# Optimization experiments

Hardware: AMD Instinct MI355X
Metric: run time of the kernel (lower is better)

## Reference

```python
import jax, jax.numpy as jnp
import numpy as np
from jax.ops import segment_sum

N = 100000   # nodes
E = 1600000  # edges
F = 128      # node feature dim
H = 128      # hidden dim
FE = 16      # edge feature dim
G = 256      # num graphs
EPS = 1e-5   # batch-norm eps


def setup_inputs() -> dict:
    key = jax.random.key(0)
    ks = jax.random.split(key, 16)
    s = 0.05
    return {
        "x": jax.random.normal(ks[0], (N, F), jnp.float32),
        "edge_index": jax.random.randint(ks[1], (2, E), 0, N, dtype=jnp.int32),
        "edge_attr": jax.random.normal(ks[2], (E, FE), jnp.float32),
        "batch_idx": jnp.sort(jax.random.randint(ks[3], (N,), 0, G, dtype=jnp.int32)),
        # GCN layer 1
        "W_g1": jax.random.normal(ks[4], (F, H), jnp.float32) * s,
        "b_g1": jnp.zeros((H,), jnp.float32),
        "gamma1": jnp.ones((H,), jnp.float32),
        "beta1": jnp.zeros((H,), jnp.float32),
        # GCN layer 2
        "W_g2": jax.random.normal(ks[5], (H, H), jnp.float32) * s,
        "b_g2": jnp.zeros((H,), jnp.float32),
        "gamma2": jnp.ones((H,), jnp.float32),
        "beta2": jnp.zeros((H,), jnp.float32),
        # edge encoder MLP
        "W_e1": jax.random.normal(ks[6], (FE, H), jnp.float32) * s,
        "b_e1": jnp.zeros((H,), jnp.float32),
        "W_e2": jax.random.normal(ks[7], (H, H), jnp.float32) * s,
        "b_e2": jnp.zeros((H,), jnp.float32),
    }


def _gcn_bn_relu(x, src, dst, W, b, gamma, beta):
    """GCNConv (sym-normalized, self-loops) + BatchNorm1d (batch stats) + ReLU."""
    h = x @ W                                             # [N, H]
    ones = jnp.ones((E,), h.dtype)
    deg = segment_sum(ones, dst, num_segments=N) + 1.0    # self-loop degree
    dinv = jax.lax.rsqrt(deg)                             # [N]
    norm = dinv[src] * dinv[dst]                          # [E]
    agg = segment_sum(h[src] * norm[:, None], dst, num_segments=N)
    out = agg + h * (dinv * dinv)[:, None] + b            # self-loop + bias
    mu = out.mean(axis=0)
    var = out.var(axis=0)
    out = (out - mu) * jax.lax.rsqrt(var + EPS) * gamma + beta
    return jax.nn.relu(out)


def reference(x, edge_index, edge_attr, batch_idx, W_g1, b_g1, gamma1, beta1,
              W_g2, b_g2, gamma2, beta2, W_e1, b_e1, W_e2, b_e2):
    src, dst = edge_index[0], edge_index[1]
    h = _gcn_bn_relu(x, src, dst, W_g1, b_g1, gamma1, beta1)
    h = _gcn_bn_relu(h, src, dst, W_g2, b_g2, gamma2, beta2)

    # global mean pool over nodes per graph
    node_cnt = segment_sum(jnp.ones((N,), h.dtype), batch_idx, num_segments=G)
    graph_repr = segment_sum(h, batch_idx, num_segments=G) / jnp.maximum(node_cnt, 1.0)[:, None]

    # edge encoder MLP + per-graph edge mean (vectorized version of the loop)
    e = jax.nn.relu(edge_attr @ W_e1 + b_e1) @ W_e2 + b_e2   # [E, H]
    edge_batch = batch_idx[src]                              # [E]
    edge_cnt = segment_sum(jnp.ones((E,), e.dtype), edge_batch, num_segments=G)
    edge_sum = segment_sum(e, edge_batch, num_segments=G)
    edge_repr = jnp.where(edge_cnt[:, None] > 0, edge_sum / jnp.maximum(edge_cnt, 1.0)[:, None], 0.0)

    return graph_repr + edge_repr  # [G, H]
```

## Files before the change

### kernel.cpp

```cpp
#include <hip/hip_runtime.h>
#include <cstdint>

__device__ inline unsigned int bfpack2(float a, float b) {
  unsigned int ua = __float_as_uint(a), ub = __float_as_uint(b);
  ua += 0x7FFFu + ((ua >> 16) & 1u);
  ub += 0x7FFFu + ((ub >> 16) & 1u);
  return (ua >> 16) | (ub & 0xFFFF0000u);
}
__device__ inline float bflo(unsigned int u) { return __uint_as_float(u << 16); }
__device__ inline float bfhi(unsigned int u) { return __uint_as_float(u & 0xFFFF0000u); }

__global__ __launch_bounds__(256) void pre_kernel(const int* __restrict__ src,
                                                  const int* __restrict__ dst,
                                                  int* __restrict__ deg,
                                                  int* __restrict__ deg2, int nE) {
  int e = blockIdx.x * 256 + threadIdx.x;
  if (e < nE) {
    atomicAdd(&deg[dst[e]], 1);
    atomicAdd(&deg2[src[e]], 1);
  }
}

__global__ __launch_bounds__(256) void scanA_kernel(const int* __restrict__ deg,
                                                    const int* __restrict__ deg2,
                                                    int* __restrict__ rp,
                                                    int* __restrict__ rp2,
                                                    int* __restrict__ part,
                                                    int* __restrict__ part2,
                                                    int n, int nb) {
  __shared__ int sh[256];
  int b = blockIdx.x, t = threadIdx.x;
  const int* d = (b < nb) ? deg : deg2;
  int* r = (b < nb) ? rp : rp2;
  int* p = (b < nb) ? part : part2;
  int pad = (b < nb) ? 1 : 0;
  int bb = (b < nb) ? b : b - nb;
  int base = bb * 1024 + t * 4;
  int v0 = (base + 0 < n) ? d[base + 0] : 0;
  int v1 = (base + 1 < n) ? d[base + 1] : 0;
  int v2 = (base + 2 < n) ? d[base + 2] : 0;
  int v3 = (base + 3 < n) ? d[base + 3] : 0;
  if (pad) {
    v0 = (v0 + 7) & ~7; v1 = (v1 + 7) & ~7;
    v2 = (v2 + 7) & ~7; v3 = (v3 + 7) & ~7;
  }
  int ts = v0 + v1 + v2 + v3;
  sh[t] = ts;
  __syncthreads();
  for (int off = 1; off < 256; off <<= 1) {
    int x = (t >= off) ? sh[t - off] : 0;
    __syncthreads();
    sh[t] += x;
    __syncthreads();
  }
  int excl = sh[t] - ts;
  if (t == 255) p[bb] = sh[255];
  if (base + 0 < n) r[base + 0] = excl;
  if (base + 1 < n) r[base + 1] = excl + v0;
  if (base + 2 < n) r[base + 2] = excl + v0 + v1;
  if (base + 3 < n) r[base + 3] = excl + v0 + v1 + v2;
}

__global__ void scanB_kernel(int* part, int* part2, int* rp, int* rp2, int nb, int n) {
  if (threadIdx.x == 0) {
    int* p = (blockIdx.x == 0) ? part : part2;
    int* r = (blockIdx.x == 0) ? rp : rp2;
    int run = 0;
    for (int i = 0; i < nb; ++i) { int v = p[i]; p[i] = run; run += v; }
    r[n] = run;
  }
}

__global__ __launch_bounds__(256) void scanC_kernel(int* __restrict__ rp,
                                                    int* __restrict__ rp2,
                                                    const int* __restrict__ part,
                                                    const int* __restrict__ part2,
                                                    int* __restrict__ cursor,
                                                    int* __restrict__ cursor2,
                                                    const int* __restrict__ deg,
                                                    float* __restrict__ dinv, int n) {
  int i = blockIdx.x * 256 + threadIdx.x;
  if (i < n) {
    int v = rp[i] + part[i >> 10];
    rp[i] = v;
    cursor[i] = v;
    dinv[i] = rsqrtf((float)deg[i] + 1.0f);
  } else if (i < 2 * n) {
    int j = i - n;
    int v = rp2[j] + part2[j >> 10];
    rp2[j] = v;
    cursor2[j] = v;
  }
}

__global__ __launch_bounds__(256) void placepad_kernel(const int* __restrict__ src,
                                                       const int* __restrict__ dst,
                                                       const int* __restrict__ batch,
                                                       const float* __restrict__ dinv,
                                                       int* __restrict__ cursor,
                                                       int* __restrict__ cursor2,
                                                       int2* __restrict__ swv,
                                                       unsigned int* __restrict__ epk,
                                                       int* __restrict__ pos2,
                                                       const int* __restrict__ rp,
                                                       const int* __restrict__ deg,
                                                       int nE, int nN) {
  int t = blockIdx.x * 256 + threadIdx.x;
  if (t < nE) {
    int s = src[t];
    int d = dst[t];
    int p1 = atomicAdd(&cursor[d], 1);
    int2 sw; sw.x = s; sw.y = __float_as_int(dinv[s] * dinv[d]);
    swv[p1] = sw;
    int g = batch[s];
    int p2 = atomicAdd(&cursor2[s], 1);
    epk[p2] = ((unsigned int)g << 21) | (unsigned int)t;
    pos2[t] = p2;
  } else if (t < nE + nN) {
    int i = t - nE;
    int b = rp[i] + deg[i], e = rp[i + 1];
    int2 z; z.x = i; z.y = 0;
    for (int k = b; k < e; ++k) swv[k] = z;
  }
}

template <bool FUSED>
__global__ __launch_bounds__(256) void gemm128_kernel(const float* __restrict__ A,
                                                      const float* __restrict__ W,
                                                      const float* __restrict__ bs,
                                                      const float* __restrict__ bq,
                                                      const float* __restrict__ gm,
                                                      const float* __restrict__ bt,
                                                      float invN,
                                                      unsigned int* __restrict__ hpk2,
                                                      int nrows) {
  extern __shared__ float lds[];
  float* Ws = lds;
  float* xs = lds + 128 * 128;
  float* scs = xs + 16 * 128;
  float* shs = scs + 128;
  const int t = threadIdx.x;
  for (int i = t; i < (128 * 128) / 4; i += 256)
    reinterpret_cast<float4*>(Ws)[i] = reinterpret_cast<const float4*>(W)[i];
  if (FUSED && t < 128) {
    float mu = bs[t] * invN;
    float var = bq[t] * invN - mu * mu;
    float sc = gm[t] * rsqrtf(var + 1e-5f);
    scs[t] = sc;
    shs[t] = bt[t] - mu * sc;
  }
  const int wave = t >> 6, lane = t & 63;
  const size_t sbase = (size_t)(lane >> 3) * (size_t)nrows * 8 + (lane & 7);
  for (int rb = blockIdx.x * 16; rb < nrows; rb += gridDim.x * 16) {
    int nr = min(16, nrows - rb);
    __syncthreads();
    for (int i = t; i < nr * 32; i += 256) {
      float4 v = reinterpret_cast<const float4*>(A + (size_t)rb * 128)[i];
      if (FUSED) {
        float4 sc4 = reinterpret_cast<const float4*>(scs)[i & 31];
        float4 sh4 = reinterpret_cast<const float4*>(shs)[i & 31];
        v.x = fmaxf(fmaf(v.x, sc4.x, sh4.x), 0.f);
        v.y = fmaxf(fmaf(v.y, sc4.y, sh4.y), 0.f);
        v.z = fmaxf(fmaf(v.z, sc4.z, sh4.z), 0.f);
        v.w = fmaxf(fmaf(v.w, sc4.w, sh4.w), 0.f);
      }
      reinterpret_cast<float4*>(xs)[i] = v;
    }
    __syncthreads();
    float acc[4][2] = {{0.f, 0.f}, {0.f, 0.f}, {0.f, 0.f}, {0.f, 0.f}};
    const float* xw = xs + wave * 4 * 128;
#pragma unroll 4
    for (int k = 0; k < 128; ++k) {
      float w0 = Ws[k * 128 + lane];
      float w1 = Ws[k * 128 + 64 + lane];
#pragma unroll
      for (int r = 0; r < 4; ++r) {
        float a = xw[r * 128 + k];
        acc[r][0] = fmaf(a, w0, acc[r][0]);
        acc[r][1] = fmaf(a, w1, acc[r][1]);
      }
    }
#pragma unroll
    for (int r = 0; r < 4; ++r) {
      int row = rb + wave * 4 + r;
      if (row < nrows)
        hpk2[sbase + (size_t)row * 8] = bfpack2(acc[r][0], acc[r][1]);
    }
  }
}

__global__ __launch_bounds__(256) void spmm8_kernel(const unsigned int* __restrict__ hpk2,
                                                    const float* __restrict__ dinv,
                                                    const int* __restrict__ rp,
                                                    const int2* __restrict__ swv,
                                                    const float* __restrict__ bias,
                                                    float* __restrict__ outp,
                                                    float* __restrict__ bnsum,
                                                    float* __restrict__ bnsq, int nN) {
  const int lane = threadIdx.x & 63;
  const int ch = lane & 7;
  const int es = lane >> 3;
  const int slice = blockIdx.x & 7;
  const unsigned int* hs = hpk2 + (size_t)slice * (size_t)nN * 8;
  const int cb = slice * 8;
  const int wib = (int)(blockIdx.x >> 3) * 4 + (int)(threadIdx.x >> 6);
  const int nws = (int)(gridDim.x >> 3) * 4;
  const unsigned long long* swq = reinterpret_cast<const unsigned long long*>(swv);
  float b0 = bias[cb + ch], b1 = bias[64 + cb + ch];
  float s0 = 0.f, s1 = 0.f, q0 = 0.f, q1 = 0.f;
  const int half = (nN + 1) >> 1;

#define SPMM_CHUNK(J, ACC0, ACC1)                                         \
  {                                                                       \
    unsigned long long v_ = __builtin_nontemporal_load(swq + (J) + es);   \
    unsigned int pp_ = hs[(size_t)(unsigned int)v_ * 8 + ch];             \
    float ww_ = __uint_as_float((unsigned int)(v_ >> 32));                \
    ACC0 = fmaf(ww_, bflo(pp_), ACC0);                                    \
    ACC1 = fmaf(ww_, bfhi(pp_), ACC1);                                    \
  }

  for (int p = wib; p < half; p += nws) {
    const int n0 = p;
    const int n1 = p + half;
    const bool has1 = n1 < nN;
    int j0 = rp[n0];
    const int end0 = rp[n0 + 1];
    int j1 = 0, end1 = 0;
    if (has1) { j1 = rp[n1]; end1 = rp[n1 + 1]; }
    float a00 = 0.f, a01 = 0.f, b00 = 0.f, b01 = 0.f;
    float a10 = 0.f, a11 = 0.f, b10 = 0.f, b11 = 0.f;
    while (j0 + 8 < end0 && j1 + 8 < end1) {
      SPMM_CHUNK(j0, a00, a01);
      SPMM_CHUNK(j0 + 8, b00, b01);
      SPMM_CHUNK(j1, a10, a11);
      SPMM_CHUNK(j1 + 8, b10, b11);
      j0 += 16; j1 += 16;
    }
    while (j0 + 8 < end0) {
      SPMM_CHUNK(j0, a00, a01);
      SPMM_CHUNK(j0 + 8, b00, b01);
      j0 += 16;
    }
    if (j0 < end0) SPMM_CHUNK(j0, a00, a01);
    while (j1 + 8 < end1) {
      SPMM_CHUNK(j1, a10, a11);
      SPMM_CHUNK(j1 + 8, b10, b11);
      j1 += 16;
    }
    if (j1 < end1) SPMM_CHUNK(j1, a10, a11);

    a00 += b00; a01 += b01;
    a10 += b10; a11 += b11;
    a00 += __shfl_xor(a00, 8);  a01 += __shfl_xor(a01, 8);
    a10 += __shfl_xor(a10, 8);  a11 += __shfl_xor(a11, 8);
    a00 += __shfl_xor(a00, 16); a01 += __shfl_xor(a01, 16);
    a10 += __shfl_xor(a10, 16); a11 += __shfl_xor(a11, 16);
    a00 += __shfl_xor(a00, 32); a01 += __shfl_xor(a01, 32);
    a10 += __shfl_xor(a10, 32); a11 += __shfl_xor(a11, 32);
    if (es == 0) {
      {
        float dn = dinv[n0];
        float sw = dn * dn;
        unsigned int pn = hs[(size_t)n0 * 8 + ch];
        float o0 = fmaf(bflo(pn), sw, a00) + b0;
        float o1 = fmaf(bfhi(pn), sw, a01) + b1;
        __builtin_nontemporal_store(o0, &outp[(size_t)n0 * 128 + cb + ch]);
        __builtin_nontemporal_store(o1, &outp[(size_t)n0 * 128 + 64 + cb + ch]);
        s0 += o0; s1 += o1;
        q0 = fmaf(o0, o0, q0); q1 = fmaf(o1, o1, q1);
      }
      if (has1) {
        float dn = dinv[n1];
        float sw = dn * dn;
        unsigned int pn = hs[(size_t)n1 * 8 + ch];
        float o0 = fmaf(bflo(pn), sw, a10) + b0;
        float o1 = fmaf(bfhi(pn), sw, a11) + b1;
        __builtin_nontemporal_store(o0, &outp[(size_t)n1 * 128 + cb + ch]);
        __builtin_nontemporal_store(o1, &outp[(size_t)n1 * 128 + 64 + cb + ch]);
        s0 += o0; s1 += o1;
        q0 = fmaf(o0, o0, q0); q1 = fmaf(o1, o1, q1);
      }
    }
  }
#undef SPMM_CHUNK
  if (es == 0) {
    atomicAdd(&bnsum[cb + ch], s0);
    atomicAdd(&bnsum[64 + cb + ch], s1);
    atomicAdd(&bnsq[cb + ch], q0);
    atomicAdd(&bnsq[64 + cb + ch], q1);
  }
}

__global__ __launch_bounds__(256) void pool_kernel(const float* __restrict__ h,
                                                   const int* __restrict__ batch,
                                                   const float* __restrict__ bs,
                                                   const float* __restrict__ bq,
                                                   const float* __restrict__ gm,
                                                   const float* __restrict__ bt,
                                                   float invN,
                                                   float* __restrict__ gsum,
                                                   float* __restrict__ gcnt,
                                                   int nN, int chunk) {
  const int lane = threadIdx.x & 63;
  const int wid = (blockIdx.x * blockDim.x + threadIdx.x) >> 6;
  int beg = wid * chunk;
  if (beg >= nN) return;
  int end = min(nN, beg + chunk);
  const int c2 = 2 * lane;
  float mu0 = bs[c2] * invN, mu1 = bs[c2 + 1] * invN;
  float va0 = bq[c2] * invN - mu0 * mu0, va1 = bq[c2 + 1] * invN - mu1 * mu1;
  float sc0 = gm[c2] * rsqrtf(va0 + 1e-5f), sc1v = gm[c2 + 1] * rsqrtf(va1 + 1e-5f);
  float sh0 = bt[c2] - mu0 * sc0, sh1v = bt[c2 + 1] - mu1 * sc1v;
  int cur = -1;
  float a0 = 0.f, a1 = 0.f, cnt = 0.f;
  for (int n = beg; n < end; ++n) {
    int g = batch[n];
    if (g != cur) {
      if (cur >= 0) {
        atomicAdd(&gsum[cur * 128 + c2], a0);
        atomicAdd(&gsum[cur * 128 + c2 + 1], a1);
        if (lane == 0) atomicAdd(&gcnt[cur], cnt);
      }
      cur = g; a0 = 0.f; a1 = 0.f; cnt = 0.f;
    }
    float2 v = *reinterpret_cast<const float2*>(h + (size_t)n * 128 + c2);
    a0 += fmaxf(fmaf(v.x, sc0, sh0), 0.f);
    a1 += fmaxf(fmaf(v.y, sc1v, sh1v), 0.f);
    cnt += 1.f;
  }
  if (cur >= 0) {
    atomicAdd(&gsum[cur * 128 + c2], a0);
    atomicAdd(&gsum[cur * 128 + c2 + 1], a1);
    if (lane == 0) atomicAdd(&gcnt[cur], cnt);
  }
}

__global__ __launch_bounds__(256) void scatter_kernel(const float* __restrict__ ea,
                                                      const int* __restrict__ pos2,
                                                      unsigned int* __restrict__ eah, int nE) {
  int e = blockIdx.x * 256 + threadIdx.x;
  if (e < nE) {
    const float4* p = reinterpret_cast<const float4*>(ea + (size_t)e * 16);
    float4 a = p[0], b = p[1], c = p[2], d = p[3];
    uint4 o0, o1;
    o0.x = bfpack2(a.x, a.y); o0.y = bfpack2(a.z, a.w);
    o0.z = bfpack2(b.x, b.y); o0.w = bfpack2(b.z, b.w);
    o1.x = bfpack2(c.x, c.y); o1.y = bfpack2(c.z, c.w);
    o1.z = bfpack2(d.x, d.y); o1.w = bfpack2(d.z, d.w);
    int j = pos2[e];
    uint4* dst = reinterpret_cast<uint4*>(eah + (size_t)j * 8);
    dst[0] = o0;
    dst[1] = o1;
  }
}

__global__ __launch_bounds__(256) void edge6_kernel(const unsigned int* __restrict__ eah,
                                                    const unsigned int* __restrict__ epk,
                                                    const float* __restrict__ We1,
                                                    const float* __restrict__ be1,
                                                    float* __restrict__ esum,
                                                    float* __restrict__ ecnt,
                                                    int nE, int chunk) {
  const int lane = threadIdx.x & 63;
  const int wid = (blockIdx.x * 256 + threadIdx.x) >> 6;
  int beg = wid * chunk;
  if (beg >= nE) return;
  int end = min(nE, beg + chunk);
  float w0[16], w1[16];
#pragma unroll
  for (int k = 0; k < 16; ++k) {
    w0[k] = We1[k * 128 + lane];
    w1[k] = We1[k * 128 + 64 + lane];
  }
  float b0 = be1[lane], b1 = be1[64 + lane];
  int cur = -1;
  float a0 = 0.f, a1 = 0.f, cnt = 0.f;
  const uint4* rowp = reinterpret_cast<const uint4*>(eah + (size_t)beg * 8);
  uint4 q0 = rowp[0], q1 = rowp[1];
  int g = (int)(epk[beg] >> 21);
  for (int j = beg; j < end; ++j) {
    uint4 n0, n1;
    int ng = g;
    if (j + 1 < end) {
      const uint4* np = reinterpret_cast<const uint4*>(eah + (size_t)(j + 1) * 8);
      n0 = np[0];
      n1 = np[1];
      ng = (int)(epk[j + 1] >> 21);
    }
    if (g != cur) {
      if (cur >= 0) {
        atomicAdd(&esum[cur * 128 + lane], a0);
        atomicAdd(&esum[cur * 128 + 64 + lane], a1);
        if (lane == 0) atomicAdd(&ecnt[cur], cnt);
      }
      cur = g; a0 = 0.f; a1 = 0.f; cnt = 0.f;
    }
    float u0 = b0, u1 = b1;
    float f;
    f = bflo(q0.x); u0 = fmaf(f, w0[0], u0);  u1 = fmaf(f, w1[0], u1);
    f = bfhi(q0.x); u0 = fmaf(f, w0[1], u0);  u1 = fmaf(f, w1[1], u1);
    f = bflo(q0.y); u0 = fmaf(f, w0[2], u0);  u1 = fmaf(f, w1[2], u1);
    f = bfhi(q0.y); u0 = fmaf(f, w0[3], u0);  u1 = fmaf(f, w1[3], u1);
    f = bflo(q0.z); u0 = fmaf(f, w0[4], u0);  u1 = fmaf(f, w1[4], u1);
    f = bfhi(q0.z); u0 = fmaf(f, w0[5], u0);  u1 = fmaf(f, w1[5], u1);
    f = bflo(q0.w); u0 = fmaf(f, w0[6], u0);  u1 = fmaf(f, w1[6], u1);
    f = bfhi(q0.w); u0 = fmaf(f, w0[7], u0);  u1 = fmaf(f, w1[7], u1);
    f = bflo(q1.x); u0 = fmaf(f, w0[8], u0);  u1 = fmaf(f, w1[8], u1);
    f = bfhi(q1.x); u0 = fmaf(f, w0[9], u0);  u1 = fmaf(f, w1[9], u1);
    f = bflo(q1.y); u0 = fmaf(f, w0[10], u0); u1 = fmaf(f, w1[10], u1);
    f = bfhi(q1.y); u0 = fmaf(f, w0[11], u0); u1 = fmaf(f, w1[11], u1);
    f = bflo(q1.z); u0 = fmaf(f, w0[12], u0); u1 = fmaf(f, w1[12], u1);
    f = bfhi(q1.z); u0 = fmaf(f, w0[13], u0); u1 = fmaf(f, w1[13], u1);
    f = bflo(q1.w); u0 = fmaf(f, w0[14], u0); u1 = fmaf(f, w1[14], u1);
    f = bfhi(q1.w); u0 = fmaf(f, w0[15], u0); u1 = fmaf(f, w1[15], u1);
    a0 += fmaxf(u0, 0.f);
    a1 += fmaxf(u1, 0.f);
    cnt += 1.f;
    q0 = n0; q1 = n1; g = ng;
  }
  if (cur >= 0) {
    atomicAdd(&esum[cur * 128 + lane], a0);
    atomicAdd(&esum[cur * 128 + 64 + lane], a1);
    if (lane == 0) atomicAdd(&ecnt[cur], cnt);
  }
}

__global__ __launch_bounds__(128) void final_kernel(const float* __restrict__ gsum,
                                                    const float* __restrict__ gcnt,
                                                    const float* __restrict__ esum,
                                                    const float* __restrict__ ecnt,
                                                    const float* __restrict__ We2,
                                                    const float* __restrict__ be2,
                                                    float* __restrict__ out) {
  __shared__ float row[128];
  int g = blockIdx.x, c = threadIdx.x;
  row[c] = esum[g * 128 + c];
  __syncthreads();
  float acc = 0.f;
#pragma unroll 4
  for (int k = 0; k < 128; ++k) acc = fmaf(row[k], We2[k * 128 + c], acc);
  float ce = ecnt[g];
  float er = (ce > 0.f) ? (acc / ce + be2[c]) : 0.f;
  float cn = gcnt[g];
  float gr = gsum[g * 128 + c] / fmaxf(cn, 1.f);
  out[g * 128 + c] = gr + er;
}

extern "C" void kernel_launch(void* const* d_in, const int* in_sizes, int n_in,
                              void* d_out, int out_size, void* d_ws, size_t ws_size,
                              hipStream_t stream) {
  const float* x    = (const float*)d_in[0];
  const int*   ei   = (const int*)d_in[1];
  const float* ea   = (const float*)d_in[2];
  const int*   bidx = (const int*)d_in[3];
  const float* Wg1  = (const float*)d_in[4];
  const float* bg1  = (const float*)d_in[5];
  const float* gm1  = (const float*)d_in[6];
  const float* bt1  = (const float*)d_in[7];
  const float* Wg2  = (const float*)d_in[8];
  const float* bg2  = (const float*)d_in[9];
  const float* gm2  = (const float*)d_in[10];
  const float* bt2  = (const float*)d_in[11];
  const float* We1  = (const float*)d_in[12];
  const float* be1  = (const float*)d_in[13];
  const float* We2  = (const float*)d_in[14];
  const float* be2  = (const float*)d_in[15];
  float* out = (float*)d_out;

  const int N = in_sizes[3];
  const int E = in_sizes[1] / 2;
  const int G = out_size / 128;
  const int* srcp = ei;
  const int* dstp = ei + E;
  const int Epad = E + 8 * N;

  char* w = (char*)d_ws;
  auto alloc = [&](size_t b) {
    char* p = w;
    w += (b + 15) & ~(size_t)15;
    return p;
  };
  float* bufB    = (float*)alloc((size_t)N * 128 * 4);
  unsigned int* hpk2 = (unsigned int*)alloc((size_t)N * 64 * 4);
  int2*  swv     = (int2*)alloc((size_t)Epad * 8);
  unsigned int* epk = (unsigned int*)alloc((size_t)E * 4);
  int*   pos2    = (int*)alloc((size_t)E * 4);
  int*   rp      = (int*)alloc((size_t)(N + 1) * 4);
  int*   rp2     = (int*)alloc((size_t)(N + 1) * 4);
  int*   cursor  = (int*)alloc((size_t)N * 4);
  int*   cursor2 = (int*)alloc((size_t)N * 4);
  float* dinv    = (float*)alloc((size_t)N * 4);
  char* zbase = w;
  int*   deg  = (int*)alloc((size_t)N * 4);
  int*   deg2 = (int*)alloc((size_t)N * 4);
  float* bs1  = (float*)alloc(512);
  float* bq1  = (float*)alloc(512);
  float* bs2  = (float*)alloc(512);
  float* bq2  = (float*)alloc(512);
  float* gsum = (float*)alloc((size_t)G * 128 * 4);
  float* gcnt = (float*)alloc((size_t)G * 4);
  float* esum = (float*)alloc((size_t)G * 128 * 4);
  float* ecnt = (float*)alloc((size_t)G * 4);
  int*   part  = (int*)alloc(4096);
  int*   part2 = (int*)alloc(4096);
  size_t zbytes = (size_t)(w - zbase);

  unsigned int* eah = (unsigned int*)bufB;

  hipMemsetAsync(zbase, 0, zbytes, stream);

  (void)hipFuncSetAttribute((const void*)gemm128_kernel<false>,
                            hipFuncAttributeMaxDynamicSharedMemorySize, 74752);
  (void)hipFuncSetAttribute((const void*)gemm128_kernel<true>,
                            hipFuncAttributeMaxDynamicSharedMemorySize, 74752);

  pre_kernel<<<(E + 255) / 256, 256, 0, stream>>>(srcp, dstp, deg, deg2, E);
  int nb = (N + 1023) / 1024;
  scanA_kernel<<<2 * nb, 256, 0, stream>>>(deg, deg2, rp, rp2, part, part2, N, nb);
  scanB_kernel<<<2, 64, 0, stream>>>(part, part2, rp, rp2, nb, N);
  scanC_kernel<<<(2 * N + 255) / 256, 256, 0, stream>>>(rp, rp2, part, part2, cursor,
                                                        cursor2, deg, dinv, N);
  placepad_kernel<<<(E + N + 255) / 256, 256, 0, stream>>>(srcp, dstp, bidx, dinv, cursor,
                                                           cursor2, swv, epk, pos2, rp, deg,
                                                           E, N);

  const float invN = 1.0f / (float)N;

  gemm128_kernel<false><<<512, 256, 74752, stream>>>(x, Wg1, nullptr, nullptr, nullptr,
                                                     nullptr, 0.f, hpk2, N);
  spmm8_kernel<<<2048, 256, 0, stream>>>(hpk2, dinv, rp, swv, bg1, bufB, bs1, bq1, N);

  gemm128_kernel<true><<<512, 256, 74752, stream>>>(bufB, Wg2, bs1, bq1, gm1, bt1, invN,
                                                    hpk2, N);
  spmm8_kernel<<<2048, 256, 0, stream>>>(hpk2, dinv, rp, swv, bg2, bufB, bs2, bq2, N);

  int nwp = (2048 * 256) / 64;
  int chunkN = (N + nwp - 1) / nwp;
  pool_kernel<<<2048, 256, 0, stream>>>(bufB, bidx, bs2, bq2, gm2, bt2, invN,
                                        gsum, gcnt, N, chunkN);

  scatter_kernel<<<(E + 255) / 256, 256, 0, stream>>>(ea, pos2, eah, E);
  int nwe = (2048 * 256) / 64;
  int chunkE = (E + nwe - 1) / nwe;
  edge6_kernel<<<2048, 256, 0, stream>>>(eah, epk, We1, be1, esum, ecnt, E, chunkE);

  final_kernel<<<G, 128, 0, stream>>>(gsum, gcnt, esum, ecnt, We2, be2, out);
}
```

Measured before the change: 1.270 ms.

## Fuse edge-attr bf16 scatter into placepad and software-pipeline SpMM index loads

The placepad kernel now converts edge attributes to bf16 and writes them straight to their src-sorted slot in a dedicated buffer, when the workspace has room. This removes the separate scatter kernel and the pos2 round trip. The SpMM main loop is software-pipelined: it prefetches the next iteration's (index, weight) pairs before the FMAs, so load latency overlaps with compute. The prefetch can read past the end of the array, so 32 extra zeroed padding slots are added to swv. The cost is a larger workspace and extra register pressure in the SpMM.

```diff
diff --git a/kernel.cpp b/kernel.cpp
--- a/kernel.cpp
+++ b/kernel.cpp
@@ -93,15 +93,18 @@
   }
 }
 
+template <bool SC>
 __global__ __launch_bounds__(256) void placepad_kernel(const int* __restrict__ src,
                                                        const int* __restrict__ dst,
                                                        const int* __restrict__ batch,
                                                        const float* __restrict__ dinv,
+                                                       const float* __restrict__ ea,
                                                        int* __restrict__ cursor,
                                                        int* __restrict__ cursor2,
                                                        int2* __restrict__ swv,
                                                        unsigned int* __restrict__ epk,
                                                        int* __restrict__ pos2,
+                                                       unsigned int* __restrict__ eah,
                                                        const int* __restrict__ rp,
                                                        const int* __restrict__ deg,
                                                        int nE, int nN) {
@@ -115,12 +118,30 @@
     int g = batch[s];
     int p2 = atomicAdd(&cursor2[s], 1);
     epk[p2] = ((unsigned int)g << 21) | (unsigned int)t;
-    pos2[t] = p2;
+    if (SC) {
+      const float4* p = reinterpret_cast<const float4*>(ea + (size_t)t * 16);
+      float4 a = p[0], b = p[1], c = p[2], dd = p[3];
+      uint4 o0, o1;
+      o0.x = bfpack2(a.x, a.y); o0.y = bfpack2(a.z, a.w);
+      o0.z = bfpack2(b.x, b.y); o0.w = bfpack2(b.z, b.w);
+      o1.x = bfpack2(c.x, c.y); o1.y = bfpack2(c.z, c.w);
+      o1.z = bfpack2(dd.x, dd.y); o1.w = bfpack2(dd.z, dd.w);
+      uint4* dp = reinterpret_cast<uint4*>(eah + (size_t)p2 * 8);
+      dp[0] = o0;
+      dp[1] = o1;
+    } else {
+      pos2[t] = p2;
+    }
   } else if (t < nE + nN) {
     int i = t - nE;
     int b = rp[i] + deg[i], e = rp[i + 1];
-    int2 z; z.x = i; z.y = 0;
+    int2 z; z.x = 0; z.y = 0;
+    z.x = i;
     for (int k = b; k < e; ++k) swv[k] = z;
+  } else if (t < nE + nN + 32) {
+    int k = t - nE - nN;
+    int2 z; z.x = 0; z.y = 0;
+    swv[rp[nN] + k] = z;
   }
 }
 
@@ -218,6 +239,12 @@
     ACC0 = fmaf(ww_, bflo(pp_), ACC0);                                    \
     ACC1 = fmaf(ww_, bfhi(pp_), ACC1);                                    \
   }
+#define SPMM_FMA(V, P, ACC0, ACC1)                                        \
+  {                                                                       \
+    float ww_ = __uint_as_float((unsigned int)((V) >> 32));               \
+    ACC0 = fmaf(ww_, bflo(P), ACC0);                                      \
+    ACC1 = fmaf(ww_, bfhi(P), ACC1);                                      \
+  }
 
   for (int p = wib; p < half; p += nws) {
     const int n0 = p;
@@ -229,12 +256,27 @@
     if (has1) { j1 = rp[n1]; end1 = rp[n1 + 1]; }
     float a00 = 0.f, a01 = 0.f, b00 = 0.f, b01 = 0.f;
     float a10 = 0.f, a11 = 0.f, b10 = 0.f, b11 = 0.f;
-    while (j0 + 8 < end0 && j1 + 8 < end1) {
-      SPMM_CHUNK(j0, a00, a01);
-      SPMM_CHUNK(j0 + 8, b00, b01);
-      SPMM_CHUNK(j1, a10, a11);
-      SPMM_CHUNK(j1 + 8, b10, b11);
+    unsigned long long v0 = __builtin_nontemporal_load(swq + j0 + es);
+    unsigned long long v1 = __builtin_nontemporal_load(swq + j0 + 8 + es);
+    unsigned long long v2 = __builtin_nontemporal_load(swq + j1 + es);
+    unsigned long long v3 = __builtin_nontemporal_load(swq + j1 + 8 + es);
+    bool run = (j0 + 8 < end0) && (j1 + 8 < end1);
+    while (run) {
+      unsigned int p0 = hs[(size_t)(unsigned int)v0 * 8 + ch];
+      unsigned int p1 = hs[(size_t)(unsigned int)v1 * 8 + ch];
+      unsigned int p2 = hs[(size_t)(unsigned int)v2 * 8 + ch];
+      unsigned int p3 = hs[(size_t)(unsigned int)v3 * 8 + ch];
       j0 += 16; j1 += 16;
+      unsigned long long n0v = __builtin_nontemporal_load(swq + j0 + es);
+      unsigned long long n1v = __builtin_nontemporal_load(swq + j0 + 8 + es);
+      unsigned long long n2v = __builtin_nontemporal_load(swq + j1 + es);
+      unsigned long long n3v = __builtin_nontemporal_load(swq + j1 + 8 + es);
+      SPMM_FMA(v0, p0, a00, a01);
+      SPMM_FMA(v1, p1, b00, b01);
+      SPMM_FMA(v2, p2, a10, a11);
+      SPMM_FMA(v3, p3, b10, b11);
+      v0 = n0v; v1 = n1v; v2 = n2v; v3 = n3v;
+      run = (j0 + 8 < end0) && (j1 + 8 < end1);
     }
     while (j0 + 8 < end0) {
       SPMM_CHUNK(j0, a00, a01);
@@ -283,6 +325,7 @@
     }
   }
 #undef SPMM_CHUNK
+#undef SPMM_FMA
   if (es == 0) {
     atomicAdd(&bnsum[cb + ch], s0);
     atomicAdd(&bnsum[64 + cb + ch], s1);
@@ -482,7 +525,7 @@
   };
   float* bufB    = (float*)alloc((size_t)N * 128 * 4);
   unsigned int* hpk2 = (unsigned int*)alloc((size_t)N * 64 * 4);
-  int2*  swv     = (int2*)alloc((size_t)Epad * 8);
+  int2*  swv     = (int2*)alloc(((size_t)Epad + 32) * 8);
   unsigned int* epk = (unsigned int*)alloc((size_t)E * 4);
   int*   pos2    = (int*)alloc((size_t)E * 4);
   int*   rp      = (int*)alloc((size_t)(N + 1) * 4);
@@ -505,7 +548,10 @@
   int*   part2 = (int*)alloc(4096);
   size_t zbytes = (size_t)(w - zbase);
 
-  unsigned int* eah = (unsigned int*)bufB;
+  size_t used = (size_t)(w - (char*)d_ws);
+  size_t eah_bytes = (size_t)E * 32;
+  bool dedicated = (used + eah_bytes + 64) <= ws_size;
+  unsigned int* eah = dedicated ? (unsigned int*)alloc(eah_bytes) : (unsigned int*)bufB;
 
   hipMemsetAsync(zbase, 0, zbytes, stream);
 
@@ -520,9 +566,16 @@
   scanB_kernel<<<2, 64, 0, stream>>>(part, part2, rp, rp2, nb, N);
   scanC_kernel<<<(2 * N + 255) / 256, 256, 0, stream>>>(rp, rp2, part, part2, cursor,
                                                         cursor2, deg, dinv, N);
-  placepad_kernel<<<(E + N + 255) / 256, 256, 0, stream>>>(srcp, dstp, bidx, dinv, cursor,
-                                                           cursor2, swv, epk, pos2, rp, deg,
-                                                           E, N);
+  int ppg = (E + N + 32 + 255) / 256;
+  if (dedicated) {
+    placepad_kernel<true><<<ppg, 256, 0, stream>>>(srcp, dstp, bidx, dinv, ea, cursor,
+                                                   cursor2, swv, epk, pos2, eah, rp, deg,
+                                                   E, N);
+  } else {
+    placepad_kernel<false><<<ppg, 256, 0, stream>>>(srcp, dstp, bidx, dinv, ea, cursor,
+                                                    cursor2, swv, epk, pos2, eah, rp, deg,
+                                                    E, N);
+  }
 
   const float invN = 1.0f / (float)N;
 
@@ -539,7 +592,9 @@
   pool_kernel<<<2048, 256, 0, stream>>>(bufB, bidx, bs2, bq2, gm2, bt2, invN,
                                         gsum, gcnt, N, chunkN);
 
-  scatter_kernel<<<(E + 255) / 256, 256, 0, stream>>>(ea, pos2, eah, E);
+  if (!dedicated) {
+    scatter_kernel<<<(E + 255) / 256, 256, 0, stream>>>(ea, pos2, eah, E);
+  }
   int nwe = (2048 * 256) / 64;
   int chunkE = (E + nwe - 1) / nwe;
   edge6_kernel<<<2048, 256, 0, stream>>>(eah, epk, We1, be1, esum, ecnt, E, chunkE);
```

Measured after the change: 1.257 ms. No clear change (-1.0%).

## Pack CSR entries into 32 bits and fuse edge-attr scatter into placement

Applied to the files above, without the earlier changes.

CSR edge entries move from an 8-byte (src, fp32 weight) pair to one 32-bit word holding a 17-bit source index and a 15-bit truncated bf16 weight, halving index traffic in both SpMM passes. When the workspace has room, edge attributes are converted to bf16 and written directly to their sorted positions inside the placement kernel, so the separate scatter kernel and the pos2 round trip are dropped. This lowers the precision of the normalization weights and limits node count to 2^17. The dedicated path also needs a larger workspace.

```diff
diff --git a/kernel.cpp b/kernel.cpp
--- a/kernel.cpp
+++ b/kernel.cpp
@@ -93,15 +93,18 @@
   }
 }
 
+template <bool SC>
 __global__ __launch_bounds__(256) void placepad_kernel(const int* __restrict__ src,
                                                        const int* __restrict__ dst,
                                                        const int* __restrict__ batch,
                                                        const float* __restrict__ dinv,
+                                                       const float* __restrict__ ea,
                                                        int* __restrict__ cursor,
                                                        int* __restrict__ cursor2,
-                                                       int2* __restrict__ swv,
+                                                       unsigned int* __restrict__ swp,
                                                        unsigned int* __restrict__ epk,
                                                        int* __restrict__ pos2,
+                                                       unsigned int* __restrict__ eah,
                                                        const int* __restrict__ rp,
                                                        const int* __restrict__ deg,
                                                        int nE, int nN) {
@@ -110,17 +113,33 @@
     int s = src[t];
     int d = dst[t];
     int p1 = atomicAdd(&cursor[d], 1);
-    int2 sw; sw.x = s; sw.y = __float_as_int(dinv[s] * dinv[d]);
-    swv[p1] = sw;
+    unsigned int fb = __float_as_uint(dinv[s] * dinv[d]);
+    fb += 0x7FFFu + ((fb >> 16) & 1u);
+    swp[p1] = ((fb >> 16) << 17) | (unsigned int)s;
     int g = batch[s];
     int p2 = atomicAdd(&cursor2[s], 1);
     epk[p2] = ((unsigned int)g << 21) | (unsigned int)t;
-    pos2[t] = p2;
+    if (SC) {
+      const float4* p = reinterpret_cast<const float4*>(ea + (size_t)t * 16);
+      float4 a = p[0], b = p[1], c = p[2], dd = p[3];
+      uint4 o0, o1;
+      o0.x = bfpack2(a.x, a.y); o0.y = bfpack2(a.z, a.w);
+      o0.z = bfpack2(b.x, b.y); o0.w = bfpack2(b.z, b.w);
+      o1.x = bfpack2(c.x, c.y); o1.y = bfpack2(c.z, c.w);
+      o1.z = bfpack2(dd.x, dd.y); o1.w = bfpack2(dd.z, dd.w);
+      uint4* dp = reinterpret_cast<uint4*>(eah + (size_t)p2 * 8);
+      dp[0] = o0;
+      dp[1] = o1;
+    } else {
+      pos2[t] = p2;
+    }
   } else if (t < nE + nN) {
     int i = t - nE;
     int b = rp[i] + deg[i], e = rp[i + 1];
-    int2 z; z.x = i; z.y = 0;
-    for (int k = b; k < e; ++k) swv[k] = z;
+    for (int k = b; k < e; ++k) swp[k] = (unsigned int)i;
+  } else if (t < nE + nN + 32) {
+    int k = t - nE - nN;
+    swp[rp[nN] + k] = 0u;
   }
 }
 
@@ -192,7 +211,7 @@
 __global__ __launch_bounds__(256) void spmm8_kernel(const unsigned int* __restrict__ hpk2,
                                                     const float* __restrict__ dinv,
                                                     const int* __restrict__ rp,
-                                                    const int2* __restrict__ swv,
+                                                    const unsigned int* __restrict__ swp,
                                                     const float* __restrict__ bias,
                                                     float* __restrict__ outp,
                                                     float* __restrict__ bnsum,
@@ -205,16 +224,15 @@
   const int cb = slice * 8;
   const int wib = (int)(blockIdx.x >> 3) * 4 + (int)(threadIdx.x >> 6);
   const int nws = (int)(gridDim.x >> 3) * 4;
-  const unsigned long long* swq = reinterpret_cast<const unsigned long long*>(swv);
   float b0 = bias[cb + ch], b1 = bias[64 + cb + ch];
   float s0 = 0.f, s1 = 0.f, q0 = 0.f, q1 = 0.f;
   const int half = (nN + 1) >> 1;
 
 #define SPMM_CHUNK(J, ACC0, ACC1)                                         \
   {                                                                       \
-    unsigned long long v_ = __builtin_nontemporal_load(swq + (J) + es);   \
-    unsigned int pp_ = hs[(size_t)(unsigned int)v_ * 8 + ch];             \
-    float ww_ = __uint_as_float((unsigned int)(v_ >> 32));                \
+    unsigned int v_ = __builtin_nontemporal_load(swp + (J) + es);         \
+    unsigned int pp_ = hs[(size_t)(v_ & 0x1FFFFu) * 8 + ch];              \
+    float ww_ = __uint_as_float((v_ & 0xFFFE0000u) >> 1);                 \
     ACC0 = fmaf(ww_, bflo(pp_), ACC0);                                    \
     ACC1 = fmaf(ww_, bfhi(pp_), ACC1);                                    \
   }
@@ -482,7 +500,7 @@
   };
   float* bufB    = (float*)alloc((size_t)N * 128 * 4);
   unsigned int* hpk2 = (unsigned int*)alloc((size_t)N * 64 * 4);
-  int2*  swv     = (int2*)alloc((size_t)Epad * 8);
+  unsigned int* swp = (unsigned int*)alloc(((size_t)Epad + 32) * 4);
   unsigned int* epk = (unsigned int*)alloc((size_t)E * 4);
   int*   pos2    = (int*)alloc((size_t)E * 4);
   int*   rp      = (int*)alloc((size_t)(N + 1) * 4);
@@ -505,7 +523,10 @@
   int*   part2 = (int*)alloc(4096);
   size_t zbytes = (size_t)(w - zbase);
 
-  unsigned int* eah = (unsigned int*)bufB;
+  size_t used = (size_t)(w - (char*)d_ws);
+  size_t eah_bytes = (size_t)E * 32;
+  bool dedicated = (used + eah_bytes + 64) <= ws_size;
+  unsigned int* eah = dedicated ? (unsigned int*)alloc(eah_bytes) : (unsigned int*)bufB;
 
   hipMemsetAsync(zbase, 0, zbytes, stream);
 
@@ -520,26 +541,35 @@
   scanB_kernel<<<2, 64, 0, stream>>>(part, part2, rp, rp2, nb, N);
   scanC_kernel<<<(2 * N + 255) / 256, 256, 0, stream>>>(rp, rp2, part, part2, cursor,
                                                         cursor2, deg, dinv, N);
-  placepad_kernel<<<(E + N + 255) / 256, 256, 0, stream>>>(srcp, dstp, bidx, dinv, cursor,
-                                                           cursor2, swv, epk, pos2, rp, deg,
-                                                           E, N);
+  int ppg = (E + N + 32 + 255) / 256;
+  if (dedicated) {
+    placepad_kernel<true><<<ppg, 256, 0, stream>>>(srcp, dstp, bidx, dinv, ea, cursor,
+                                                   cursor2, swp, epk, pos2, eah, rp, deg,
+                                                   E, N);
+  } else {
+    placepad_kernel<false><<<ppg, 256, 0, stream>>>(srcp, dstp, bidx, dinv, ea, cursor,
+                                                    cursor2, swp, epk, pos2, eah, rp, deg,
+                                                    E, N);
+  }
 
   const float invN = 1.0f / (float)N;
 
   gemm128_kernel<false><<<512, 256, 74752, stream>>>(x, Wg1, nullptr, nullptr, nullptr,
                                                      nullptr, 0.f, hpk2, N);
-  spmm8_kernel<<<2048, 256, 0, stream>>>(hpk2, dinv, rp, swv, bg1, bufB, bs1, bq1, N);
+  spmm8_kernel<<<2048, 256, 0, stream>>>(hpk2, dinv, rp, swp, bg1, bufB, bs1, bq1, N);
 
   gemm128_kernel<true><<<512, 256, 74752, stream>>>(bufB, Wg2, bs1, bq1, gm1, bt1, invN,
                                                     hpk2, N);
-  spmm8_kernel<<<2048, 256, 0, stream>>>(hpk2, dinv, rp, swv, bg2, bufB, bs2, bq2, N);
+  spmm8_kernel<<<2048, 256, 0, stream>>>(hpk2, dinv, rp, swp, bg2, bufB, bs2, bq2, N);
 
   int nwp = (2048 * 256) / 64;
   int chunkN = (N + nwp - 1) / nwp;
   pool_kernel<<<2048, 256, 0, stream>>>(bufB, bidx, bs2, bq2, gm2, bt2, invN,
                                         gsum, gcnt, N, chunkN);
 
-  scatter_kernel<<<(E + 255) / 256, 256, 0, stream>>>(ea, pos2, eah, E);
+  if (!dedicated) {
+    scatter_kernel<<<(E + 255) / 256, 256, 0, stream>>>(ea, pos2, eah, E);
+  }
   int nwe = (2048 * 256) / 64;
   int chunkE = (E + nwe - 1) / nwe;
   edge6_kernel<<<2048, 256, 0, stream>>>(eah, epk, We1, be1, esum, ecnt, E, chunkE);
```

New measurement: 1.236 ms (median of 2 runs). 2.6% less time.
